# Optimization experiments

Measured on AMD Instinct MI355X. Metric: run time of the kernel, lower is better.

Reference implementation:

```python
import jax, jax.numpy as jnp
import numpy as np

DIM = 32
DEPTH = 2  # closed-form Lyndon-basis log-signature implemented for depth 2


def setup_inputs() -> dict:
    key = jax.random.key(0)
    B, L, D = 512, 2048, DIM
    x = jax.random.normal(key, (B, L, D), dtype=jnp.float32)
    return {"x": x}


def _logsig_depth2(x):
    # x: (B, L, D) batch of paths.
    dx = x[:, 1:, :] - x[:, :-1, :]                     # (B, L-1, D) increments
    prefix = jnp.cumsum(dx, axis=1)                      # inclusive prefix sums
    level1 = prefix[:, -1, :]                            # (B, D) total displacement
    prefix_excl = prefix - dx                            # prefix up to t-1 (exclusive)
    # level-2 signature S_ij = sum_t prefix_excl[t, i] * dx[t, j]  -> (B, D, D)
    S2 = jnp.einsum("bli,blj->bij", prefix_excl, dx)
    # log-signature level 2 = antisymmetric part (Levy areas), Lyndon words i<j
    A = 0.5 * (S2 - jnp.swapaxes(S2, 1, 2))             # (B, D, D)
    iu, ju = jnp.triu_indices(x.shape[-1], k=1)          # row-major upper triangle
    areas = A[:, iu, ju]                                 # (B, D*(D-1)/2)
    return jnp.concatenate([level1, areas], axis=-1)     # (B, D + D*(D-1)/2)


def reference(x):
    # Faithful batched equivalent of iisignature.logsig(path, prepare(dim, 2))
    # for every path in the batch (Lyndon basis, depth 2).
    return _logsig_depth2(x)
```

## Files before the change

### kernel.cpp

```cpp
#include <hip/hip_runtime.h>
#include <stdint.h>


constexpr int kB   = 512;
constexpr int kL   = 2048;
constexpr int kD   = 32;
constexpr int kOut = 528;
constexpr int kPan = 32;
constexpr int kTw  = 256;
constexpr int kNP  = kTw / kPan;
constexpr int kCh  = 264;
constexpr int kPB  = 4 * kCh;

typedef __attribute__((ext_vector_type(8))) short bfrag;
typedef __attribute__((ext_vector_type(4))) float f4acc;
union FragU { uint32_t u[4]; bfrag f; };

#if defined(__has_builtin)
#if __has_builtin(__builtin_amdgcn_global_load_lds)
#define LOGSIG_ASYNC_LDS 1
#endif
#endif

__device__ __forceinline__ void async_ld16(const uint32_t* g, uint32_t* l, int lane) {
#ifdef LOGSIG_ASYNC_LDS
    auto* gp = reinterpret_cast<const __attribute__((address_space(1))) uint32_t*>(
        reinterpret_cast<uintptr_t>(g));
    auto* lp = reinterpret_cast<__attribute__((address_space(3))) uint32_t*>(
        reinterpret_cast<uintptr_t>(l));
    __builtin_amdgcn_global_load_lds(gp, lp, 16, 0, 0);
#else
    *(float4*)(l + lane * 4) = *(const float4*)g;
#endif
}

__global__ __launch_bounds__(256, 4)
void logsig_mfma(const float* __restrict__ x, float* __restrict__ out) {
    __shared__ __align__(16) uint32_t sStage[4][2][kPB];
    __shared__ float sx0[kD], sL1[kD];

    const int b     = blockIdx.x >> 1;
    const int chunk = blockIdx.x & 1;
    const int tid   = threadIdx.x;
    const int wave  = tid >> 6;
    const int lane  = tid & 63;
    const int m     = lane & 15;
    const int q     = lane >> 4;

    const float* __restrict__ xb = x + (size_t)b * (kL * kD);
    const int t0w = chunk * 1024 + wave * kTw;

    auto stage_panel = [&](int p, int buf) {
        uint32_t* dst = &sStage[wave][buf][0];
        const int rbase = t0w + p * kPan;
        #pragma unroll
        for (int c = 0; c < 4; ++c) {
            int r = rbase + c * 8 + (lane >> 3);
            r = r < kL - 1 ? r : kL - 1;
            const uint32_t* g = (const uint32_t*)xb + (size_t)r * kD + (lane & 7) * 4;
            async_ld16(g, dst + c * kCh, lane);
        }
    };

    f4acc acc[4];
    #pragma unroll
    for (int t = 0; t < 4; ++t)
        #pragma unroll
        for (int e = 0; e < 4; ++e) acc[t][e] = 0.0f;

    auto make_frags = [&](const uint32_t* e, FragU& AH, FragU& AL,
                          FragU& BH, FragU& BL) {
        uint32_t l[9];
        #pragma unroll
        for (int j = 0; j < 9; ++j) {
            const uint32_t fh = e[j] & 0xffff0000u;
            const float r = __builtin_bit_cast(float, e[j])
                          - __builtin_bit_cast(float, fh);
            l[j] = __builtin_bit_cast(uint32_t, r);
        }
        #pragma unroll
        for (int d = 0; d < 4; ++d) {
            AH.u[d] = __builtin_amdgcn_perm(e[2*d+1], e[2*d],   0x07060302u);
            AL.u[d] = __builtin_amdgcn_perm(l[2*d+1], l[2*d],   0x07060302u);
            BH.u[d] = __builtin_amdgcn_perm(e[2*d+2], e[2*d+1], 0x07060302u);
            BL.u[d] = __builtin_amdgcn_perm(l[2*d+2], l[2*d+1], 0x07060302u);
        }
    };

    stage_panel(0, 0);

    #pragma unroll
    for (int p = 0; p < kNP; ++p) {
        const int cu = p & 1, nb = cu ^ 1;

        uint32_t h0 = 0, h1 = 0;
        if (p == kNP - 1) {
            int hr = t0w + kTw;
            hr = hr < kL - 1 ? hr : kL - 1;
            const uint32_t* g = (const uint32_t*)xb + (size_t)hr * kD;
            h0 = g[m];
            h1 = g[m + 16];
        }

        if (p + 1 < kNP) {
            stage_panel(p + 1, nb);
            asm volatile("s_waitcnt vmcnt(3)" ::: "memory");
        } else {
            asm volatile("s_waitcnt vmcnt(0)" ::: "memory");
        }

        const uint32_t* sb = &sStage[wave][cu][0];
        uint32_t e0[9], e1[9];
        #pragma unroll
        for (int j = 0; j < 8; ++j) {
            const int a = q * kCh + j * 32 + m;
            e0[j] = sb[a];
            e1[j] = sb[a + 16];
        }
        if (p == kNP - 1 && q == 3) {
            e0[8] = h0;
            e1[8] = h1;
        } else {
            const uint32_t* hb = (q < 3) ? sb + (q + 1) * kCh
                                         : &sStage[wave][nb][0];
            e0[8] = hb[m];
            e1[8] = hb[m + 16];
        }

        FragU A0H, A0L, B0H, B0L, A1H, A1L, B1H, B1L;
        make_frags(e0, A0H, A0L, B0H, B0L);
        make_frags(e1, A1H, A1L, B1H, B1L);

        acc[0] = __builtin_amdgcn_mfma_f32_16x16x32_bf16(A0H.f, B0H.f, acc[0], 0, 0, 0);
        acc[0] = __builtin_amdgcn_mfma_f32_16x16x32_bf16(A0H.f, B0L.f, acc[0], 0, 0, 0);
        acc[0] = __builtin_amdgcn_mfma_f32_16x16x32_bf16(A0L.f, B0H.f, acc[0], 0, 0, 0);
        acc[1] = __builtin_amdgcn_mfma_f32_16x16x32_bf16(A0H.f, B1H.f, acc[1], 0, 0, 0);
        acc[1] = __builtin_amdgcn_mfma_f32_16x16x32_bf16(A0H.f, B1L.f, acc[1], 0, 0, 0);
        acc[1] = __builtin_amdgcn_mfma_f32_16x16x32_bf16(A0L.f, B1H.f, acc[1], 0, 0, 0);
        acc[2] = __builtin_amdgcn_mfma_f32_16x16x32_bf16(A1H.f, B0H.f, acc[2], 0, 0, 0);
        acc[2] = __builtin_amdgcn_mfma_f32_16x16x32_bf16(A1H.f, B0L.f, acc[2], 0, 0, 0);
        acc[2] = __builtin_amdgcn_mfma_f32_16x16x32_bf16(A1L.f, B0H.f, acc[2], 0, 0, 0);
        acc[3] = __builtin_amdgcn_mfma_f32_16x16x32_bf16(A1H.f, B1H.f, acc[3], 0, 0, 0);
        acc[3] = __builtin_amdgcn_mfma_f32_16x16x32_bf16(A1H.f, B1L.f, acc[3], 0, 0, 0);
        acc[3] = __builtin_amdgcn_mfma_f32_16x16x32_bf16(A1L.f, B1H.f, acc[3], 0, 0, 0);
    }

    float* sWw = (float*)&sStage[wave][0][0];
    #pragma unroll
    for (int t = 0; t < 4; ++t) {
        const int tr = t >> 1, tc = t & 1;
        #pragma unroll
        for (int e = 0; e < 4; ++e) {
            const int row = 16 * tr + q * 4 + e;
            const int col = 16 * tc + m;
            sWw[row * kD + col] = acc[t][e];
        }
    }
    if (tid < kD) {
        const float x0v = xb[tid];
        const float xev = xb[(size_t)(kL - 1) * kD + tid];
        sx0[tid] = x0v;
        sL1[tid] = xev - x0v;
    }
    __syncthreads();

    float* sW0 = (float*)&sStage[0][0][0];
    for (int c = tid; c < kD * kD; c += 256)
        sW0[c] += ((float*)&sStage[1][0][0])[c]
                + ((float*)&sStage[2][0][0])[c]
                + ((float*)&sStage[3][0][0])[c];
    __syncthreads();

    float* ob = out + (size_t)b * kOut;
    for (int o = tid; o < kOut; o += 256) {
        if (o < 32) {
            if (chunk == 0) ob[o] = sL1[o];
        } else {
            int p = o - 32, i = 0;
            while (p >= 31 - i) { p -= 31 - i; ++i; }
            const int j = i + 1 + p;
            float v = 0.5f * (sW0[i * kD + j] - sW0[j * kD + i]);
            if (chunk == 0)
                v += 0.5f * (sx0[j] * sL1[i] - sx0[i] * sL1[j]);
            atomicAdd(ob + o, v);
        }
    }
}

extern "C" void kernel_launch(void* const* d_in, const int* in_sizes, int n_in,
                              void* d_out, int out_size, void* d_ws, size_t ws_size,
                              hipStream_t stream) {
    const float* x = (const float*)d_in[0];
    float* out = (float*)d_out;
    hipMemsetAsync(out, 0, (size_t)out_size * sizeof(float), stream);
    logsig_mfma<<<dim3(kB * 2), dim3(256), 0, stream>>>(x, out);
}
```

Baseline: 189.4 us.

## Use one block per path with triple-buffered staging and drop atomics/memset

Each block now processes a whole path (512 timesteps per wave) instead of splitting it across two blocks. The staging ring grows from two to three LDS buffers so two panels are in flight at once. Because there is no longer a cross-block reduction, the memset and the atomicAdd are removed and the output is written directly. In exchange the grid halves to 512 blocks, launch bounds drop to 2 blocks per CU and LDS use rises, which lowers occupancy and parallelism on a large GPU.

Result: no change. 190.2 us (+0.4%).

```diff
diff --git a/kernel.cpp b/kernel.cpp
--- a/kernel.cpp
+++ b/kernel.cpp
@@ -7,7 +7,7 @@
 constexpr int kD   = 32;
 constexpr int kOut = 528;
 constexpr int kPan = 32;
-constexpr int kTw  = 256;
+constexpr int kTw  = 512;
 constexpr int kNP  = kTw / kPan;
 constexpr int kCh  = 264;
 constexpr int kPB  = 4 * kCh;
@@ -34,29 +34,27 @@
 #endif
 }
 
-__global__ __launch_bounds__(256, 4)
+__global__ __launch_bounds__(256, 2)
 void logsig_mfma(const float* __restrict__ x, float* __restrict__ out) {
-    __shared__ __align__(16) uint32_t sStage[4][2][kPB];
+    __shared__ __align__(16) uint32_t sStage[4][3][kPB];
     __shared__ float sx0[kD], sL1[kD];
 
-    const int b     = blockIdx.x >> 1;
-    const int chunk = blockIdx.x & 1;
-    const int tid   = threadIdx.x;
-    const int wave  = tid >> 6;
-    const int lane  = tid & 63;
-    const int m     = lane & 15;
-    const int q     = lane >> 4;
+    const int b    = blockIdx.x;
+    const int tid  = threadIdx.x;
+    const int wave = tid >> 6;
+    const int lane = tid & 63;
+    const int m    = lane & 15;
+    const int q    = lane >> 4;
 
     const float* __restrict__ xb = x + (size_t)b * (kL * kD);
-    const int t0w = chunk * 1024 + wave * kTw;
+    const int t0w = wave * kTw;
 
     auto stage_panel = [&](int p, int buf) {
         uint32_t* dst = &sStage[wave][buf][0];
         const int rbase = t0w + p * kPan;
         #pragma unroll
         for (int c = 0; c < 4; ++c) {
-            int r = rbase + c * 8 + (lane >> 3);
-            r = r < kL - 1 ? r : kL - 1;
+            const int r = rbase + c * 8 + (lane >> 3);
             const uint32_t* g = (const uint32_t*)xb + (size_t)r * kD + (lane & 7) * 4;
             async_ld16(g, dst + c * kCh, lane);
         }
@@ -88,11 +86,10 @@
     };
 
     stage_panel(0, 0);
+    stage_panel(1, 1);
 
     #pragma unroll
     for (int p = 0; p < kNP; ++p) {
-        const int cu = p & 1, nb = cu ^ 1;
-
         uint32_t h0 = 0, h1 = 0;
         if (p == kNP - 1) {
             int hr = t0w + kTw;
@@ -102,14 +99,16 @@
             h1 = g[m + 16];
         }
 
-        if (p + 1 < kNP) {
-            stage_panel(p + 1, nb);
+        if (p + 2 < kNP) {
+            stage_panel(p + 2, (p + 2) % 3);
+            asm volatile("s_waitcnt vmcnt(7)" ::: "memory");
+        } else if (p + 1 < kNP) {
             asm volatile("s_waitcnt vmcnt(3)" ::: "memory");
         } else {
             asm volatile("s_waitcnt vmcnt(0)" ::: "memory");
         }
 
-        const uint32_t* sb = &sStage[wave][cu][0];
+        const uint32_t* sb = &sStage[wave][p % 3][0];
         uint32_t e0[9], e1[9];
         #pragma unroll
         for (int j = 0; j < 8; ++j) {
@@ -117,14 +116,17 @@
             e0[j] = sb[a];
             e1[j] = sb[a + 16];
         }
-        if (p == kNP - 1 && q == 3) {
+        if (q < 3) {
+            const int a8 = (q + 1) * kCh + m;
+            e0[8] = sb[a8];
+            e1[8] = sb[a8 + 16];
+        } else if (p + 1 < kNP) {
+            const uint32_t* nbuf = &sStage[wave][(p + 1) % 3][0];
+            e0[8] = nbuf[m];
+            e1[8] = nbuf[m + 16];
+        } else {
             e0[8] = h0;
             e1[8] = h1;
-        } else {
-            const uint32_t* hb = (q < 3) ? sb + (q + 1) * kCh
-                                         : &sStage[wave][nb][0];
-            e0[8] = hb[m];
-            e1[8] = hb[m + 16];
         }
 
         FragU A0H, A0L, B0H, B0L, A1H, A1L, B1H, B1L;
@@ -174,15 +176,13 @@
     float* ob = out + (size_t)b * kOut;
     for (int o = tid; o < kOut; o += 256) {
         if (o < 32) {
-            if (chunk == 0) ob[o] = sL1[o];
+            ob[o] = sL1[o];
         } else {
             int p = o - 32, i = 0;
             while (p >= 31 - i) { p -= 31 - i; ++i; }
             const int j = i + 1 + p;
-            float v = 0.5f * (sW0[i * kD + j] - sW0[j * kD + i]);
-            if (chunk == 0)
-                v += 0.5f * (sx0[j] * sL1[i] - sx0[i] * sL1[j]);
-            atomicAdd(ob + o, v);
+            ob[o] = 0.5f * (sW0[i * kD + j] - sW0[j * kD + i]
+                            + sx0[j] * sL1[i] - sx0[i] * sL1[j]);
         }
     }
 }
@@ -192,6 +192,5 @@
                               hipStream_t stream) {
     const float* x = (const float*)d_in[0];
     float* out = (float*)d_out;
-    hipMemsetAsync(out, 0, (size_t)out_size * sizeof(float), stream);
-    logsig_mfma<<<dim3(kB * 2), dim3(256), 0, stream>>>(x, out);
+    logsig_mfma<<<dim3(kB), dim3(256), 0, stream>>>(x, out);
 }
```
